# Kernel tuning notes

Measured on AMD Instinct MI355X. Metric: run time of the kernel, lower is better.

The kernel has to match this reference:

```python
import jax, jax.numpy as jnp
import numpy as np

VOCAB, EMB, FEAT = 30000, 300, 2048
B, NQ, NW, NK = 256, 32, 12, 64


def setup_inputs() -> dict:
    key = jax.random.key(0)
    ks = jax.random.split(key, 10)
    return {
        "wv": jax.random.normal(ks[0], (VOCAB, EMB), jnp.float32),
        "Wf": jax.random.normal(ks[1], (EMB, FEAT), jnp.float32) * 0.02,
        "bf": jax.random.normal(ks[2], (EMB,), jnp.float32) * 0.02,
        "Wp": jax.random.normal(ks[3], (EMB, EMB), jnp.float32) * 0.05,
        "bp": jax.random.normal(ks[4], (EMB,), jnp.float32) * 0.02,
        "Wm": jax.random.normal(ks[5], (EMB, EMB), jnp.float32) * 0.05,
        "bm": jax.random.normal(ks[6], (EMB,), jnp.float32) * 0.02,
        "feature": jax.random.normal(ks[7], (B, NK, FEAT), jnp.float32),
        "query": jax.random.randint(ks[8], (B, NQ, NW), 0, VOCAB),
        "label": jax.random.randint(ks[9], (B, NK), 0, VOCAB),
    }


def reference(wv, Wf, bf, Wp, bp, Wm, bm, feature, query, label):
    # Dropouts act as identity in eval mode.
    eps = 1e-5
    q_emb = wv[query]                                   # [B, queries, words, D]
    k_emb = wv[label] + feature @ Wf.T + bf             # [B, objects, D]
    scale = 1.0 / np.sqrt(EMB)
    att = jnp.einsum('byqd,bkd->byqk', q_emb, k_emb) * scale
    att = jax.nn.softmax(att, axis=-1)                  # over objects
    q_max_att = jnp.max(att, axis=3)                    # [B, queries, words]
    neg_inf = -jnp.finfo(q_max_att.dtype).max
    q_max_att = jnp.where(query == 0, neg_inf, q_max_att)
    q_max_norm_att = jax.nn.softmax(q_max_att, axis=-1) / 5.0
    p_emb = jnp.einsum('byq,byqd->byd', q_max_norm_att, q_emb)  # [B, queries, D]
    p_emb = (p_emb @ Wp.T + bp) + eps * (p_emb @ Wm.T + bm)
    return p_emb, k_emb
```

## Files before the change

kernel.cpp:

```cpp
#include <hip/hip_runtime.h>

typedef unsigned short u16;
typedef unsigned int u32;
typedef __bf16 bf16x8 __attribute__((ext_vector_type(8)));
typedef float f32x4 __attribute__((ext_vector_type(4)));

#if defined(__has_builtin)
#  if __has_builtin(__builtin_amdgcn_cvt_pk_bf16_f32)
#    define PK_BF16 1
#  endif
#endif

__device__ __forceinline__ u16 f2bu(float f){
  u32 u = __float_as_uint(f);
  return (u16)((u + 0x7fffu + ((u >> 16) & 1u)) >> 16);
}
__device__ __forceinline__ float b2f(u16 u){
  union { float f; u32 i; } v; v.i = ((u32)u) << 16; return v.f;
}
__device__ __forceinline__ u32 pkbf(float a, float b){
#ifdef PK_BF16
  typedef __bf16 bf16x2 __attribute__((ext_vector_type(2)));
  union { bf16x2 h; u32 u; } c;
  c.h = __builtin_amdgcn_cvt_pk_bf16_f32(a, b);
  return c.u;
#else
  return (u32)f2bu(a) | ((u32)f2bu(b) << 16);
#endif
}
__device__ __forceinline__ void glds16(const u16* g, u16* l){
  __builtin_amdgcn_global_load_lds(
      (const __attribute__((address_space(1))) void*)g,
      (__attribute__((address_space(3))) void*)l, 16, 0, 0);
}

__global__ __launch_bounds__(256) void prep_wc(
    const float* __restrict__ Wp, const float* __restrict__ bp,
    const float* __restrict__ Wm, const float* __restrict__ bm,
    u16* __restrict__ Wc, float* __restrict__ bc)
{
  int idx = blockIdx.x * 256 + threadIdx.x;
  if (idx < 384 * 160) {
    int n = idx / 160, k = (idx % 160) * 2;
    float v0 = 0.f, v1 = 0.f;
    if (n < 300 && k < 300) {
      v0 = Wp[n * 300 + k]     + 1e-5f * Wm[n * 300 + k];
      v1 = Wp[n * 300 + k + 1] + 1e-5f * Wm[n * 300 + k + 1];
    }
    ((u32*)Wc)[idx] = pkbf(v0, v1);
    if (idx < 384) bc[idx] = (idx < 300) ? bp[idx] + 1e-5f * bm[idx] : 0.f;
  }
}

__global__ __launch_bounds__(256) void prep_wv16(
    const float* __restrict__ wv, u16* __restrict__ wv16)
{
  int idx = blockIdx.x * 256 + threadIdx.x;
  if (idx < 30000 * 160) {
    int row = idx / 160, k = (idx % 160) * 2;
    float v0 = 0.f, v1 = 0.f;
    if (k < 300) {
      v0 = wv[(size_t)row * 300 + k];
      v1 = wv[(size_t)row * 300 + k + 1];
    }
    ((u32*)wv16)[idx] = pkbf(v0, v1);
  }
}

__global__ __launch_bounds__(256) void prep_f16(
    const float* __restrict__ src, u16* __restrict__ dst, int n4)
{
  int i = blockIdx.x * 256 + threadIdx.x;
  if (i < n4) {
    float4 v = ((const float4*)src)[i];
    uint2 o; o.x = pkbf(v.x, v.y); o.y = pkbf(v.z, v.w);
    ((uint2*)dst)[i] = o;
  }
}

__global__ __launch_bounds__(256) void prep_wf16(
    const float* __restrict__ Wf, u16* __restrict__ Wf16)
{
  int i = blockIdx.x * 256 + threadIdx.x;
  if (i < 384 * 1024) {
    int row = i >> 10, c2 = (i & 1023) * 2;
    float v0 = 0.f, v1 = 0.f;
    if (row < 300) {
      v0 = Wf[(size_t)row * 2048 + c2];
      v1 = Wf[(size_t)row * 2048 + c2 + 1];
    }
    ((u32*)Wf16)[i] = pkbf(v0, v1);
  }
}

template <int GLDS>
__global__ __launch_bounds__(256) void gemm0_kernel(
    const float* __restrict__ A, const float* __restrict__ B,
    const u16* __restrict__ Af16, const u16* __restrict__ Bf16,
    const float* __restrict__ bias,
    const int* __restrict__ label, const float* __restrict__ wv,
    float* __restrict__ C, u16* __restrict__ kemb16)
{
  __shared__ __align__(16) u16 As[128 * 32];
  __shared__ __align__(16) u16 Bs[128 * 32];
  const int lda = 2048, K = 2048, nbn = 3, nsrc = 300;
  int t = threadIdx.x;
  int bm = (blockIdx.x / nbn) * 128;
  int bn = (blockIdx.x % nbn) * 128;
  int lane = t & 63, w = t >> 6;
  int wm = (w >> 1) * 64, wn = (w & 1) * 64;

  f32x4 acc[4][4];
  for (int i = 0; i < 4; i++)
    for (int j = 0; j < 4; j++)
      for (int r = 0; r < 4; r++) acc[i][j][r] = 0.f;

  int mrow = lane & 15, q = lane >> 4;

  for (int kk = 0; kk < K; kk += 32) {
    if (GLDS) {
      int r0 = w * 32;
      int rl = lane >> 2, ch = lane & 3;
      #pragma unroll
      for (int p = 0; p < 2; p++) {
        int row = r0 + p * 16 + rl;
        glds16(&Af16[(size_t)(bm + row) * 2048 + kk + ch * 8],
               &As[(r0 + p * 16) * 32]);
        glds16(&Bf16[(size_t)(bn + row) * 2048 + kk + ch * 8],
               &Bs[(r0 + p * 16) * 32]);
      }
    } else {
      #pragma unroll
      for (int p = 0; p < 2; p++) {
        int idx = t + p * 256;
        int row = idx >> 2, ch = idx & 3;
        int brow = bn + row;
        if (brow >= nsrc) brow = 0;
        const float4* ap = (const float4*)&A[(size_t)(bm + row) * lda + kk + ch * 8];
        float4 a0 = ap[0], a1 = ap[1];
        const float4* bpp = (const float4*)&B[(size_t)brow * lda + kk + ch * 8];
        float4 b0 = bpp[0], b1 = bpp[1];
        union { u32 u[4]; uint4 v; } pa, pb;
        pa.u[0] = pkbf(a0.x, a0.y); pa.u[1] = pkbf(a0.z, a0.w);
        pa.u[2] = pkbf(a1.x, a1.y); pa.u[3] = pkbf(a1.z, a1.w);
        pb.u[0] = pkbf(b0.x, b0.y); pb.u[1] = pkbf(b0.z, b0.w);
        pb.u[2] = pkbf(b1.x, b1.y); pb.u[3] = pkbf(b1.z, b1.w);
        *(uint4*)&As[idx * 8] = pa.v;
        *(uint4*)&Bs[idx * 8] = pb.v;
      }
    }
    __syncthreads();

    bf16x8 af[4], bfr[4];
    #pragma unroll
    for (int i = 0; i < 4; i++)
      af[i] = *(const bf16x8*)&As[(wm + i * 16 + mrow) * 32 + q * 8];
    #pragma unroll
    for (int j = 0; j < 4; j++)
      bfr[j] = *(const bf16x8*)&Bs[(wn + j * 16 + mrow) * 32 + q * 8];
    #pragma unroll
    for (int i = 0; i < 4; i++)
      #pragma unroll
      for (int j = 0; j < 4; j++)
        acc[i][j] = __builtin_amdgcn_mfma_f32_16x16x32_bf16(
            af[i], bfr[j], acc[i][j], 0, 0, 0);
    __syncthreads();
  }

  #pragma unroll
  for (int i = 0; i < 4; i++)
    #pragma unroll
    for (int j = 0; j < 4; j++) {
      int col = bn + wn + j * 16 + (lane & 15);
      int rb = bm + wm + i * 16 + (lane >> 4) * 4;
      #pragma unroll
      for (int r = 0; r < 4; r++) {
        int m = rb + r;
        if (col < 300) {
          float v = acc[i][j][r];
          v += bias[col] + wv[(size_t)label[m] * 300 + col];
          C[(size_t)m * 300 + col] = v;
          if (kemb16) kemb16[(size_t)m * 320 + col] = f2bu(v);
        } else if (kemb16 && col < 320) {
          kemb16[(size_t)m * 320 + col] = 0;
        }
      }
    }
}

#define KES 344
template <int FULL>
__global__ __launch_bounds__(256) void attn_kernel(
    const float* __restrict__ wv, const u16* __restrict__ wv16,
    const int* __restrict__ query,
    const float* __restrict__ kout, const u16* __restrict__ kemb16,
    u16* __restrict__ praw)
{
  __shared__ __align__(16) u16 ke[64 * KES];
  __shared__ __align__(16) int qoff[192];
  __shared__ __align__(16) float awd[192];
  __shared__ __align__(16) float wt[192];

  int blk = blockIdx.x, b = blk >> 1, bh = blk & 1;
  int t = threadIdx.x;
  int lane = t & 63, w = t >> 6;

  if (FULL) {
    for (int i = t; i < 2560; i += 256) {
      int row = i / 40, ch = i % 40;
      *(uint4*)&ke[row * KES + ch * 8] =
          *(const uint4*)&kemb16[(size_t)(b * 64 + row) * 320 + ch * 8];
    }
  } else {
    for (int i = t; i < 4800; i += 256) {
      int row = i / 75, c4 = i % 75;
      float4 v = *(const float4*)&kout[(size_t)(b * 64 + row) * 300 + c4 * 4];
      *(u32*)&ke[row * KES + c4 * 4]     = pkbf(v.x, v.y);
      *(u32*)&ke[row * KES + c4 * 4 + 2] = pkbf(v.z, v.w);
    }
    for (int i = t; i < 640; i += 256) {
      int row = i / 10, c2 = i % 10;
      *(u32*)&ke[row * KES + 300 + c2 * 2] = 0;
    }
  }
  if (t < 192)
    qoff[t] = query[b * 384 + bh * 192 + t] * (FULL ? 320 : 300);
  __syncthreads();

  int mrow = lane & 15, q = lane >> 4;
  f32x4 acc[3][4];
  #pragma unroll
  for (int i = 0; i < 3; i++)
    #pragma unroll
    for (int j = 0; j < 4; j++)
      #pragma unroll
      for (int r = 0; r < 4; r++) acc[i][j][r] = 0.f;

  int base[3];
  #pragma unroll
  for (int i = 0; i < 3; i++) base[i] = qoff[w * 48 + i * 16 + mrow];
  int keb = mrow * KES + q * 8;

  bf16x8 afn[3];
  #pragma unroll
  for (int i = 0; i < 3; i++) {
    if (FULL)
      afn[i] = *(const bf16x8*)&wv16[(size_t)base[i] + q * 8];
  }

  for (int k0 = 0; k0 < 320; k0 += 32) {
    bf16x8 af[3], bfr[4];
    #pragma unroll
    for (int i = 0; i < 3; i++) {
      if (FULL) {
        af[i] = afn[i];
        if (k0 + 32 < 320)
          afn[i] = *(const bf16x8*)&wv16[(size_t)base[i] + k0 + 32 + q * 8];
      } else {
        int cs = k0 + q * 8;
        union { u32 u[4]; bf16x8 h; } c;
        if (cs + 8 <= 300) {
          const float4* p = (const float4*)&wv[(size_t)base[i] + cs];
          float4 x = p[0], y = p[1];
          c.u[0] = pkbf(x.x, x.y); c.u[1] = pkbf(x.z, x.w);
          c.u[2] = pkbf(y.x, y.y); c.u[3] = pkbf(y.z, y.w);
        } else if (cs < 300) {
          float4 x = *(const float4*)&wv[(size_t)base[i] + 296];
          c.u[0] = pkbf(x.x, x.y); c.u[1] = pkbf(x.z, x.w);
          c.u[2] = 0; c.u[3] = 0;
        } else {
          c.u[0] = 0; c.u[1] = 0; c.u[2] = 0; c.u[3] = 0;
        }
        af[i] = c.h;
      }
    }
    #pragma unroll
    for (int j = 0; j < 4; j++)
      bfr[j] = *(const bf16x8*)&ke[j * 16 * KES + keb + k0];
    #pragma unroll
    for (int i = 0; i < 3; i++)
      #pragma unroll
      for (int j = 0; j < 4; j++)
        acc[i][j] = __builtin_amdgcn_mfma_f32_16x16x32_bf16(
            af[i], bfr[j], acc[i][j], 0, 0, 0);
  }

  const float scale = 0.05773502691896258f;
  #pragma unroll
  for (int i = 0; i < 3; i++)
    #pragma unroll
    for (int r = 0; r < 4; r++) {
      float mx = fmaxf(fmaxf(acc[i][0][r], acc[i][1][r]),
                       fmaxf(acc[i][2][r], acc[i][3][r]));
      #pragma unroll
      for (int d = 1; d < 16; d <<= 1)
        mx = fmaxf(mx, __shfl_xor(mx, d));
      float se = 0.f;
      #pragma unroll
      for (int j = 0; j < 4; j++)
        se += __expf((acc[i][j][r] - mx) * scale);
      #pragma unroll
      for (int d = 1; d < 16; d <<= 1)
        se += __shfl_xor(se, d);
      if (mrow == 0) {
        int wl = w * 48 + i * 16 + q * 4 + r;
        awd[wl] = (qoff[wl] == 0) ? -3.402823466e38f : (1.0f / se);
      }
    }
  __syncthreads();

  if (t < 16) {
    int yb = t * 12;
    float m2 = -3.402823466e38f;
    for (int i = 0; i < 12; i++) m2 = fmaxf(m2, awd[yb + i]);
    float e[12], s2 = 0.f;
    for (int i = 0; i < 12; i++) { e[i] = __expf(awd[yb + i] - m2); s2 += e[i]; }
    float inv = 0.2f / s2;
    for (int i = 0; i < 12; i++) wt[yb + i] = e[i] * inv;
  }
  __syncthreads();

  #pragma unroll
  for (int yy = 0; yy < 4; yy++) {
    int yl = w * 4 + yy;
    int row = b * 32 + bh * 16 + yl;
    if (FULL) {
      if (lane < 40) {
        float s[8];
        #pragma unroll
        for (int e = 0; e < 8; e++) s[e] = 0.f;
        for (int i = 0; i < 12; i++) {
          float g = wt[yl * 12 + i];
          union { uint4 v; u16 h[8]; } qv;
          qv.v = *(const uint4*)&wv16[(size_t)qoff[yl * 12 + i] + lane * 8];
          #pragma unroll
          for (int e = 0; e < 8; e++) s[e] += g * b2f(qv.h[e]);
        }
        union { uint4 v; u16 h[8]; } o;
        #pragma unroll
        for (int e = 0; e < 8; e++) o.h[e] = f2bu(s[e]);
        *(uint4*)&praw[(size_t)row * 320 + lane * 8] = o.v;
      }
    } else {
      #pragma unroll
      for (int c = 0; c < 5; c++) {
        int d = c * 64 + lane;
        float s = 0.f;
        if (d < 300)
          for (int i = 0; i < 12; i++)
            s += wt[yl * 12 + i] * wv[(size_t)qoff[yl * 12 + i] + d];
        praw[(size_t)row * 320 + d] = f2bu(s);
      }
    }
  }
}

__global__ __launch_bounds__(256) void proj_kernel(
    const u16* __restrict__ praw, const u16* __restrict__ Wc,
    const float* __restrict__ bc, float* __restrict__ P)
{
  __shared__ __align__(16) u16 As[128 * 32];
  __shared__ __align__(16) u16 Bs[128 * 32];
  int t = threadIdx.x;
  int bm = (blockIdx.x / 3) * 128;
  int bn = (blockIdx.x % 3) * 128;
  int lane = t & 63, w = t >> 6;
  int wm = (w >> 1) * 64, wn = (w & 1) * 64;

  f32x4 acc[4][4];
  for (int i = 0; i < 4; i++)
    for (int j = 0; j < 4; j++)
      for (int r = 0; r < 4; r++) acc[i][j][r] = 0.f;

  int mrow = lane & 15, q = lane >> 4;

  for (int kk = 0; kk < 320; kk += 32) {
    int r0 = w * 32;
    int rl = lane >> 2, ch = lane & 3;
    #pragma unroll
    for (int p = 0; p < 2; p++) {
      int row = r0 + p * 16 + rl;
      glds16(&praw[(size_t)(bm + row) * 320 + kk + ch * 8],
             &As[(r0 + p * 16) * 32]);
      glds16(&Wc[(size_t)(bn + row) * 320 + kk + ch * 8],
             &Bs[(r0 + p * 16) * 32]);
    }
    __syncthreads();

    bf16x8 af[4], bfr[4];
    #pragma unroll
    for (int i = 0; i < 4; i++)
      af[i] = *(const bf16x8*)&As[(wm + i * 16 + mrow) * 32 + q * 8];
    #pragma unroll
    for (int j = 0; j < 4; j++)
      bfr[j] = *(const bf16x8*)&Bs[(wn + j * 16 + mrow) * 32 + q * 8];
    #pragma unroll
    for (int i = 0; i < 4; i++)
      #pragma unroll
      for (int j = 0; j < 4; j++)
        acc[i][j] = __builtin_amdgcn_mfma_f32_16x16x32_bf16(
            af[i], bfr[j], acc[i][j], 0, 0, 0);
    __syncthreads();
  }

  #pragma unroll
  for (int i = 0; i < 4; i++)
    #pragma unroll
    for (int j = 0; j < 4; j++) {
      int col = bn + wn + j * 16 + (lane & 15);
      if (col >= 300) continue;
      int rb = bm + wm + i * 16 + (lane >> 4) * 4;
      #pragma unroll
      for (int r = 0; r < 4; r++)
        P[(size_t)(rb + r) * 300 + col] = acc[i][j][r] + bc[col];
    }
}

extern "C" void kernel_launch(void* const* d_in, const int* in_sizes, int n_in,
                              void* d_out, int out_size, void* d_ws,
                              size_t ws_size, hipStream_t stream)
{
  const float* wv      = (const float*)d_in[0];
  const float* Wf      = (const float*)d_in[1];
  const float* bf      = (const float*)d_in[2];
  const float* Wp      = (const float*)d_in[3];
  const float* bp      = (const float*)d_in[4];
  const float* Wm      = (const float*)d_in[5];
  const float* bm      = (const float*)d_in[6];
  const float* feature = (const float*)d_in[7];
  const int*   query   = (const int*)d_in[8];
  const int*   label   = (const int*)d_in[9];

  float* out   = (float*)d_out;
  float* p_out = out;
  float* k_out = out + 2457600;

  char* ws = (char*)d_ws;
  int t2 = ws_size >= (size_t)103857664;
  int t1 = ws_size >= (size_t)35175936;
  u16 *f16 = 0, *wf16 = 0, *wv16 = 0, *kemb16 = 0, *praw, *Wc;
  float* bc;
  if (t2) {
    f16    = (u16*)ws;
    wv16   = (u16*)(ws + 67108864);
    kemb16 = (u16*)(ws + 86308864);
    praw   = (u16*)(ws + 96794624);
    Wc     = (u16*)(ws + 102037504);
    wf16   = (u16*)(ws + 102283264);
    bc     = (float*)(ws + 103856128);
  } else if (t1) {
    wv16   = (u16*)ws;
    kemb16 = (u16*)(ws + 19200000);
    praw   = (u16*)(ws + 29685760);
    Wc     = (u16*)(ws + 34928640);
    bc     = (float*)(ws + 35174400);
  } else {
    praw   = (u16*)ws;
    Wc     = (u16*)(ws + 5242880);
    bc     = (float*)(ws + 5488640);
  }

  prep_wc<<<240, 256, 0, stream>>>(Wp, bp, Wm, bm, Wc, bc);
  if (t1 || t2)
    prep_wv16<<<18750, 256, 0, stream>>>(wv, wv16);
  if (t2) {
    prep_f16<<<32768, 256, 0, stream>>>(feature, f16, 8388608);
    prep_wf16<<<1536, 256, 0, stream>>>(Wf, wf16);
    gemm0_kernel<1><<<384, 256, 0, stream>>>(feature, Wf, f16, wf16, bf,
                                             label, wv, k_out, kemb16);
  } else {
    gemm0_kernel<0><<<384, 256, 0, stream>>>(feature, Wf, 0, 0, bf,
                                             label, wv, k_out, kemb16);
  }

  if (t1 || t2)
    attn_kernel<1><<<512, 256, 0, stream>>>(wv, wv16, query, k_out,
                                            kemb16, praw);
  else
    attn_kernel<0><<<512, 256, 0, stream>>>(wv, wv16, query, k_out,
                                            kemb16, praw);

  proj_kernel<<<192, 256, 0, stream>>>(praw, Wc, bc, p_out);
}
```

Before: 376.8 us.

## Load fp32 features directly to LDS in double-buffered GEMM, drop bf16 prep pass

Removes the separate kernel that converted the 64MB feature tensor to bf16. A new GEMM kernel streams fp32 feature tiles straight into LDS via global_load_lds with an XOR swizzle, converts them to bf16 while building MFMA fragments, and double-buffers the A/B tiles. It also uses 64x128 tiles with a remapped block order across 768 blocks. This removes a full read-plus-write pass over the feature tensor, at the cost of more LDS traffic and in-loop conversion work.

```diff
diff --git a/kernel.cpp b/kernel.cpp
--- a/kernel.cpp
+++ b/kernel.cpp
@@ -33,6 +33,11 @@
       (const __attribute__((address_space(1))) void*)g,
       (__attribute__((address_space(3))) void*)l, 16, 0, 0);
 }
+__device__ __forceinline__ void glds16f(const float* g, float* l){
+  __builtin_amdgcn_global_load_lds(
+      (const __attribute__((address_space(1))) void*)g,
+      (__attribute__((address_space(3))) void*)l, 16, 0, 0);
+}
 
 __global__ __launch_bounds__(256) void prep_wc(
     const float* __restrict__ Wp, const float* __restrict__ bp,
@@ -64,17 +69,6 @@
       v1 = wv[(size_t)row * 300 + k + 1];
     }
     ((u32*)wv16)[idx] = pkbf(v0, v1);
-  }
-}
-
-__global__ __launch_bounds__(256) void prep_f16(
-    const float* __restrict__ src, u16* __restrict__ dst, int n4)
-{
-  int i = blockIdx.x * 256 + threadIdx.x;
-  if (i < n4) {
-    float4 v = ((const float4*)src)[i];
-    uint2 o; o.x = pkbf(v.x, v.y); o.y = pkbf(v.z, v.w);
-    ((uint2*)dst)[i] = o;
   }
 }
 
@@ -118,36 +112,23 @@
   int mrow = lane & 15, q = lane >> 4;
 
   for (int kk = 0; kk < K; kk += 32) {
-    if (GLDS) {
-      int r0 = w * 32;
-      int rl = lane >> 2, ch = lane & 3;
-      #pragma unroll
-      for (int p = 0; p < 2; p++) {
-        int row = r0 + p * 16 + rl;
-        glds16(&Af16[(size_t)(bm + row) * 2048 + kk + ch * 8],
-               &As[(r0 + p * 16) * 32]);
-        glds16(&Bf16[(size_t)(bn + row) * 2048 + kk + ch * 8],
-               &Bs[(r0 + p * 16) * 32]);
-      }
-    } else {
-      #pragma unroll
-      for (int p = 0; p < 2; p++) {
-        int idx = t + p * 256;
-        int row = idx >> 2, ch = idx & 3;
-        int brow = bn + row;
-        if (brow >= nsrc) brow = 0;
-        const float4* ap = (const float4*)&A[(size_t)(bm + row) * lda + kk + ch * 8];
-        float4 a0 = ap[0], a1 = ap[1];
-        const float4* bpp = (const float4*)&B[(size_t)brow * lda + kk + ch * 8];
-        float4 b0 = bpp[0], b1 = bpp[1];
-        union { u32 u[4]; uint4 v; } pa, pb;
-        pa.u[0] = pkbf(a0.x, a0.y); pa.u[1] = pkbf(a0.z, a0.w);
-        pa.u[2] = pkbf(a1.x, a1.y); pa.u[3] = pkbf(a1.z, a1.w);
-        pb.u[0] = pkbf(b0.x, b0.y); pb.u[1] = pkbf(b0.z, b0.w);
-        pb.u[2] = pkbf(b1.x, b1.y); pb.u[3] = pkbf(b1.z, b1.w);
-        *(uint4*)&As[idx * 8] = pa.v;
-        *(uint4*)&Bs[idx * 8] = pb.v;
-      }
+    #pragma unroll
+    for (int p = 0; p < 2; p++) {
+      int idx = t + p * 256;
+      int row = idx >> 2, ch = idx & 3;
+      int brow = bn + row;
+      if (brow >= nsrc) brow = 0;
+      const float4* ap = (const float4*)&A[(size_t)(bm + row) * lda + kk + ch * 8];
+      float4 a0 = ap[0], a1 = ap[1];
+      const float4* bpp = (const float4*)&B[(size_t)brow * lda + kk + ch * 8];
+      float4 b0 = bpp[0], b1 = bpp[1];
+      union { u32 u[4]; uint4 v; } pa, pb;
+      pa.u[0] = pkbf(a0.x, a0.y); pa.u[1] = pkbf(a0.z, a0.w);
+      pa.u[2] = pkbf(a1.x, a1.y); pa.u[3] = pkbf(a1.z, a1.w);
+      pb.u[0] = pkbf(b0.x, b0.y); pb.u[1] = pkbf(b0.z, b0.w);
+      pb.u[2] = pkbf(b1.x, b1.y); pb.u[3] = pkbf(b1.z, b1.w);
+      *(uint4*)&As[idx * 8] = pa.v;
+      *(uint4*)&Bs[idx * 8] = pb.v;
     }
     __syncthreads();
 
@@ -182,6 +163,102 @@
           C[(size_t)m * 300 + col] = v;
           if (kemb16) kemb16[(size_t)m * 320 + col] = f2bu(v);
         } else if (kemb16 && col < 320) {
+          kemb16[(size_t)m * 320 + col] = 0;
+        }
+      }
+    }
+}
+
+__global__ __launch_bounds__(256) void gemm0v3_kernel(
+    const float* __restrict__ A, const u16* __restrict__ Bf16,
+    const float* __restrict__ bias, const int* __restrict__ label,
+    const float* __restrict__ wv, float* __restrict__ C,
+    u16* __restrict__ kemb16)
+{
+  __shared__ __align__(16) float As[2][64 * 32];
+  __shared__ __align__(16) u16  Bs[2][128 * 32];
+  const int NIT = 64;
+  int t = threadIdx.x;
+  int g = blockIdx.x;
+  int seq = (g & 7) * 96 + (g >> 3);
+  int bm = (seq / 3) * 64;
+  int bn = (seq % 3) * 128;
+  int lane = t & 63, w = t >> 6;
+  int wm = (w >> 1) * 32, wn = (w & 1) * 64;
+
+  f32x4 acc[2][4];
+  #pragma unroll
+  for (int i = 0; i < 2; i++)
+    #pragma unroll
+    for (int j = 0; j < 4; j++)
+      #pragma unroll
+      for (int r = 0; r < 4; r++) acc[i][j][r] = 0.f;
+
+  int mrow = lane & 15, q = lane >> 4;
+  int rlA = lane >> 3, chA = lane & 7;
+  int rlB = lane >> 2, chB = lane & 3;
+  int csA = (chA ^ rlA) * 4;
+  int csB = chB * 8;
+
+  const float* gA0 = &A[(size_t)(bm + w * 16 + rlA) * 2048 + csA];
+  const float* gA1 = &A[(size_t)(bm + w * 16 + 8 + rlA) * 2048 + csA];
+  const u16*   gB0 = &Bf16[(size_t)(bn + w * 32 + rlB) * 2048 + csB];
+  const u16*   gB1 = &Bf16[(size_t)(bn + w * 32 + 16 + rlB) * 2048 + csB];
+
+  auto STAGE = [&](int buf, int kk) {
+    glds16f(gA0 + kk, &As[buf][(w * 16) * 32]);
+    glds16f(gA1 + kk, &As[buf][(w * 16 + 8) * 32]);
+    glds16(gB0 + kk, &Bs[buf][(w * 32) * 32]);
+    glds16(gB1 + kk, &Bs[buf][(w * 32 + 16) * 32]);
+  };
+
+  STAGE(0, 0);
+  __syncthreads();
+
+  for (int it = 0; it < NIT; ++it) {
+    int cur = it & 1;
+    if (it + 1 < NIT) STAGE(cur ^ 1, (it + 1) * 32);
+
+    bf16x8 af[2], bfr[4];
+    #pragma unroll
+    for (int i = 0; i < 2; i++) {
+      int r = wm + i * 16 + mrow;
+      int c0 = ((q * 2) ^ (r & 7)) * 4;
+      int c1 = ((q * 2 + 1) ^ (r & 7)) * 4;
+      f32x4 x = *(const f32x4*)&As[cur][r * 32 + c0];
+      f32x4 y = *(const f32x4*)&As[cur][r * 32 + c1];
+      union { u32 u[4]; bf16x8 h; } cc;
+      cc.u[0] = pkbf(x[0], x[1]); cc.u[1] = pkbf(x[2], x[3]);
+      cc.u[2] = pkbf(y[0], y[1]); cc.u[3] = pkbf(y[2], y[3]);
+      af[i] = cc.h;
+    }
+    #pragma unroll
+    for (int j = 0; j < 4; j++)
+      bfr[j] = *(const bf16x8*)&Bs[cur][(wn + j * 16 + mrow) * 32 + q * 8];
+    #pragma unroll
+    for (int i = 0; i < 2; i++)
+      #pragma unroll
+      for (int j = 0; j < 4; j++)
+        acc[i][j] = __builtin_amdgcn_mfma_f32_16x16x32_bf16(
+            af[i], bfr[j], acc[i][j], 0, 0, 0);
+
+    __syncthreads();
+  }
+
+  #pragma unroll
+  for (int i = 0; i < 2; i++)
+    #pragma unroll
+    for (int j = 0; j < 4; j++) {
+      int col = bn + wn + j * 16 + (lane & 15);
+      int rb = bm + wm + i * 16 + (lane >> 4) * 4;
+      #pragma unroll
+      for (int r = 0; r < 4; r++) {
+        int m = rb + r;
+        if (col < 300) {
+          float v = acc[i][j][r] + bias[col] + wv[(size_t)label[m] * 300 + col];
+          C[(size_t)m * 300 + col] = v;
+          kemb16[(size_t)m * 320 + col] = f2bu(v);
+        } else if (col < 320) {
           kemb16[(size_t)m * 320 + col] = 0;
         }
       }
@@ -438,10 +515,9 @@
   char* ws = (char*)d_ws;
   int t2 = ws_size >= (size_t)103857664;
   int t1 = ws_size >= (size_t)35175936;
-  u16 *f16 = 0, *wf16 = 0, *wv16 = 0, *kemb16 = 0, *praw, *Wc;
+  u16 *wf16 = 0, *wv16 = 0, *kemb16 = 0, *praw, *Wc;
   float* bc;
   if (t2) {
-    f16    = (u16*)ws;
     wv16   = (u16*)(ws + 67108864);
     kemb16 = (u16*)(ws + 86308864);
     praw   = (u16*)(ws + 96794624);
@@ -464,10 +540,9 @@
   if (t1 || t2)
     prep_wv16<<<18750, 256, 0, stream>>>(wv, wv16);
   if (t2) {
-    prep_f16<<<32768, 256, 0, stream>>>(feature, f16, 8388608);
     prep_wf16<<<1536, 256, 0, stream>>>(Wf, wf16);
-    gemm0_kernel<1><<<384, 256, 0, stream>>>(feature, Wf, f16, wf16, bf,
-                                             label, wv, k_out, kemb16);
+    gemm0v3_kernel<<<768, 256, 0, stream>>>(feature, wf16, bf,
+                                            label, wv, k_out, kemb16);
   } else {
     gemm0_kernel<0><<<384, 256, 0, stream>>>(feature, Wf, 0, 0, bf,
                                              label, wv, k_out, kemb16);
```

Result: faster. 353.0 us (-6.3%).

## Drop feature bf16 prepass; stream fp32 A directly into MFMA registers without LDS

Applied to the files above, without the earlier changes.

Removes the separate kernel that converted the whole 64MB feature tensor to bf16 and rewrites the k-embedding GEMM to load fp32 feature rows straight from global memory, converting to bf16 in registers and feeding MFMA without shared-memory staging. Tiles become 128x64 with an XCD-aware block mapping so each XCD covers contiguous M rows across all six N tiles, sharing A in its L2. This cuts one full read and write of the large activation. In exchange each wave redundantly fetches its B fragments from global or cache memory, with no LDS reuse.

```diff
diff --git a/kernel.cpp b/kernel.cpp
--- a/kernel.cpp
+++ b/kernel.cpp
@@ -67,17 +67,6 @@
   }
 }
 
-__global__ __launch_bounds__(256) void prep_f16(
-    const float* __restrict__ src, u16* __restrict__ dst, int n4)
-{
-  int i = blockIdx.x * 256 + threadIdx.x;
-  if (i < n4) {
-    float4 v = ((const float4*)src)[i];
-    uint2 o; o.x = pkbf(v.x, v.y); o.y = pkbf(v.z, v.w);
-    ((uint2*)dst)[i] = o;
-  }
-}
-
 __global__ __launch_bounds__(256) void prep_wf16(
     const float* __restrict__ Wf, u16* __restrict__ Wf16)
 {
@@ -118,36 +107,23 @@
   int mrow = lane & 15, q = lane >> 4;
 
   for (int kk = 0; kk < K; kk += 32) {
-    if (GLDS) {
-      int r0 = w * 32;
-      int rl = lane >> 2, ch = lane & 3;
-      #pragma unroll
-      for (int p = 0; p < 2; p++) {
-        int row = r0 + p * 16 + rl;
-        glds16(&Af16[(size_t)(bm + row) * 2048 + kk + ch * 8],
-               &As[(r0 + p * 16) * 32]);
-        glds16(&Bf16[(size_t)(bn + row) * 2048 + kk + ch * 8],
-               &Bs[(r0 + p * 16) * 32]);
-      }
-    } else {
-      #pragma unroll
-      for (int p = 0; p < 2; p++) {
-        int idx = t + p * 256;
-        int row = idx >> 2, ch = idx & 3;
-        int brow = bn + row;
-        if (brow >= nsrc) brow = 0;
-        const float4* ap = (const float4*)&A[(size_t)(bm + row) * lda + kk + ch * 8];
-        float4 a0 = ap[0], a1 = ap[1];
-        const float4* bpp = (const float4*)&B[(size_t)brow * lda + kk + ch * 8];
-        float4 b0 = bpp[0], b1 = bpp[1];
-        union { u32 u[4]; uint4 v; } pa, pb;
-        pa.u[0] = pkbf(a0.x, a0.y); pa.u[1] = pkbf(a0.z, a0.w);
-        pa.u[2] = pkbf(a1.x, a1.y); pa.u[3] = pkbf(a1.z, a1.w);
-        pb.u[0] = pkbf(b0.x, b0.y); pb.u[1] = pkbf(b0.z, b0.w);
-        pb.u[2] = pkbf(b1.x, b1.y); pb.u[3] = pkbf(b1.z, b1.w);
-        *(uint4*)&As[idx * 8] = pa.v;
-        *(uint4*)&Bs[idx * 8] = pb.v;
-      }
+    #pragma unroll
+    for (int p = 0; p < 2; p++) {
+      int idx = t + p * 256;
+      int row = idx >> 2, ch = idx & 3;
+      int brow = bn + row;
+      if (brow >= nsrc) brow = 0;
+      const float4* ap = (const float4*)&A[(size_t)(bm + row) * lda + kk + ch * 8];
+      float4 a0 = ap[0], a1 = ap[1];
+      const float4* bpp = (const float4*)&B[(size_t)brow * lda + kk + ch * 8];
+      float4 b0 = bpp[0], b1 = bpp[1];
+      union { u32 u[4]; uint4 v; } pa, pb;
+      pa.u[0] = pkbf(a0.x, a0.y); pa.u[1] = pkbf(a0.z, a0.w);
+      pa.u[2] = pkbf(a1.x, a1.y); pa.u[3] = pkbf(a1.z, a1.w);
+      pb.u[0] = pkbf(b0.x, b0.y); pb.u[1] = pkbf(b0.z, b0.w);
+      pb.u[2] = pkbf(b1.x, b1.y); pb.u[3] = pkbf(b1.z, b1.w);
+      *(uint4*)&As[idx * 8] = pa.v;
+      *(uint4*)&Bs[idx * 8] = pb.v;
     }
     __syncthreads();
 
@@ -182,6 +158,85 @@
           C[(size_t)m * 300 + col] = v;
           if (kemb16) kemb16[(size_t)m * 320 + col] = f2bu(v);
         } else if (kemb16 && col < 320) {
+          kemb16[(size_t)m * 320 + col] = 0;
+        }
+      }
+    }
+}
+
+__global__ __launch_bounds__(256, 4) void gemm0v4_kernel(
+    const float* __restrict__ A, const u16* __restrict__ Bf16,
+    const float* __restrict__ bias, const int* __restrict__ label,
+    const float* __restrict__ wv, float* __restrict__ C,
+    u16* __restrict__ kemb16)
+{
+  int t = threadIdx.x;
+  int lane = t & 63, w = t >> 6;
+  int g = blockIdx.x;
+  int xcd = g & 7, loc = g >> 3;
+  int mloc = loc / 6, nn = loc % 6;
+  int bm = (xcd * 16 + mloc) * 128;
+  int bn = nn * 64;
+  int mrow = lane & 15, q = lane >> 4;
+  int wm = w * 32;
+
+  f32x4 acc[2][4];
+  #pragma unroll
+  for (int i = 0; i < 2; i++)
+    #pragma unroll
+    for (int j = 0; j < 4; j++)
+      #pragma unroll
+      for (int r = 0; r < 4; r++) acc[i][j][r] = 0.f;
+
+  const float* pa0 = &A[(size_t)(bm + wm + mrow) * 2048 + q * 8];
+  const float* pa1 = pa0 + (size_t)16 * 2048;
+  const u16*   pb0 = &Bf16[(size_t)(bn + mrow) * 2048 + q * 8];
+  const u16*   pb1 = pb0 + (size_t)16 * 2048;
+  const u16*   pb2 = pb0 + (size_t)32 * 2048;
+  const u16*   pb3 = pb0 + (size_t)48 * 2048;
+
+  for (int kk = 0; kk < 2048; kk += 256) {
+    #pragma unroll
+    for (int s = 0; s < 8; s++) {
+      int off = kk + s * 32;
+      f32x4 a00 = *(const f32x4*)(pa0 + off);
+      f32x4 a01 = *(const f32x4*)(pa0 + off + 4);
+      f32x4 a10 = *(const f32x4*)(pa1 + off);
+      f32x4 a11 = *(const f32x4*)(pa1 + off + 4);
+      bf16x8 b0 = *(const bf16x8*)(pb0 + off);
+      bf16x8 b1 = *(const bf16x8*)(pb1 + off);
+      bf16x8 b2 = *(const bf16x8*)(pb2 + off);
+      bf16x8 b3 = *(const bf16x8*)(pb3 + off);
+      union { u32 u[4]; bf16x8 h; } fa0, fa1;
+      fa0.u[0] = pkbf(a00[0], a00[1]); fa0.u[1] = pkbf(a00[2], a00[3]);
+      fa0.u[2] = pkbf(a01[0], a01[1]); fa0.u[3] = pkbf(a01[2], a01[3]);
+      fa1.u[0] = pkbf(a10[0], a10[1]); fa1.u[1] = pkbf(a10[2], a10[3]);
+      fa1.u[2] = pkbf(a11[0], a11[1]); fa1.u[3] = pkbf(a11[2], a11[3]);
+      acc[0][0] = __builtin_amdgcn_mfma_f32_16x16x32_bf16(fa0.h, b0, acc[0][0], 0, 0, 0);
+      acc[0][1] = __builtin_amdgcn_mfma_f32_16x16x32_bf16(fa0.h, b1, acc[0][1], 0, 0, 0);
+      acc[0][2] = __builtin_amdgcn_mfma_f32_16x16x32_bf16(fa0.h, b2, acc[0][2], 0, 0, 0);
+      acc[0][3] = __builtin_amdgcn_mfma_f32_16x16x32_bf16(fa0.h, b3, acc[0][3], 0, 0, 0);
+      acc[1][0] = __builtin_amdgcn_mfma_f32_16x16x32_bf16(fa1.h, b0, acc[1][0], 0, 0, 0);
+      acc[1][1] = __builtin_amdgcn_mfma_f32_16x16x32_bf16(fa1.h, b1, acc[1][1], 0, 0, 0);
+      acc[1][2] = __builtin_amdgcn_mfma_f32_16x16x32_bf16(fa1.h, b2, acc[1][2], 0, 0, 0);
+      acc[1][3] = __builtin_amdgcn_mfma_f32_16x16x32_bf16(fa1.h, b3, acc[1][3], 0, 0, 0);
+    }
+  }
+
+  #pragma unroll
+  for (int i = 0; i < 2; i++)
+    #pragma unroll
+    for (int j = 0; j < 4; j++) {
+      int col = bn + j * 16 + (lane & 15);
+      int rb = bm + wm + i * 16 + (lane >> 4) * 4;
+      #pragma unroll
+      for (int r = 0; r < 4; r++) {
+        int m = rb + r;
+        if (col < 300) {
+          float v = acc[i][j][r] + bias[col] + wv[(size_t)label[m] * 300 + col];
+          C[(size_t)m * 300 + col] = v;
+          kemb16[(size_t)m * 320 + col] = f2bu(v);
+        } else if (col < 320) {
           kemb16[(size_t)m * 320 + col] = 0;
         }
       }
@@ -438,10 +493,9 @@
   char* ws = (char*)d_ws;
   int t2 = ws_size >= (size_t)103857664;
   int t1 = ws_size >= (size_t)35175936;
-  u16 *f16 = 0, *wf16 = 0, *wv16 = 0, *kemb16 = 0, *praw, *Wc;
+  u16 *wf16 = 0, *wv16 = 0, *kemb16 = 0, *praw, *Wc;
   float* bc;
   if (t2) {
-    f16    = (u16*)ws;
     wv16   = (u16*)(ws + 67108864);
     kemb16 = (u16*)(ws + 86308864);
     praw   = (u16*)(ws + 96794624);
@@ -464,10 +518,9 @@
   if (t1 || t2)
     prep_wv16<<<18750, 256, 0, stream>>>(wv, wv16);
   if (t2) {
-    prep_f16<<<32768, 256, 0, stream>>>(feature, f16, 8388608);
     prep_wf16<<<1536, 256, 0, stream>>>(Wf, wf16);
-    gemm0_kernel<1><<<384, 256, 0, stream>>>(feature, Wf, f16, wf16, bf,
-                                             label, wv, k_out, kemb16);
+    gemm0v4_kernel<<<768, 256, 0, stream>>>(feature, wf16, bf,
+                                            label, wv, k_out, kemb16);
   } else {
     gemm0_kernel<0><<<384, 256, 0, stream>>>(feature, Wf, 0, 0, bf,
                                              label, wv, k_out, kemb16);
```

Result: slower. 450.2 us (+19.5%).
